# Kernel optimization log

Measured on AMD Instinct MI355X. Metric: run time of the kernel, lower is better.

## Reference

```python
import jax, jax.numpy as jnp
import numpy as np

N = 50000
E = 800000
D = 128
EPS = 1e-5


def setup_inputs() -> dict:
    key = jax.random.key(0)
    ks = jax.random.split(key, 12)
    s1 = 1.0 / np.sqrt(2 * D)
    s2 = 1.0 / np.sqrt(D)
    return {
        "x": jax.random.normal(ks[0], (N, D), dtype=jnp.float32),
        "edge_index": jax.random.randint(ks[1], (2, E), 0, N, dtype=jnp.int32),
        # message MLP: Linear(2D->D), SiLU, Linear(D->D)
        "wm1": jax.random.uniform(ks[2], (2 * D, D), jnp.float32, -s1, s1),
        "bm1": jax.random.uniform(ks[3], (D,), jnp.float32, -s1, s1),
        "wm2": jax.random.uniform(ks[4], (D, D), jnp.float32, -s2, s2),
        "bm2": jax.random.uniform(ks[5], (D,), jnp.float32, -s2, s2),
        # update MLP: Linear(2D->D), SiLU, Linear(D->D)
        "wu1": jax.random.uniform(ks[6], (2 * D, D), jnp.float32, -s1, s1),
        "bu1": jax.random.uniform(ks[7], (D,), jnp.float32, -s1, s1),
        "wu2": jax.random.uniform(ks[8], (D, D), jnp.float32, -s2, s2),
        "bu2": jax.random.uniform(ks[9], (D,), jnp.float32, -s2, s2),
        # LayerNorm affine
        "gamma": jnp.ones((D,), jnp.float32),
        "beta": jnp.zeros((D,), jnp.float32),
    }


def reference(x, edge_index, wm1, bm1, wm2, bm2, wu1, bu1, wu2, bu2, gamma, beta):
    row, col = edge_index[0], edge_index[1]
    # gather endpoints and build message input [E, 2D]
    msg_in = jnp.concatenate([x[row], x[col]], axis=-1)
    h = jax.nn.silu(msg_in @ wm1 + bm1)
    messages = h @ wm2 + bm2  # [E, D]
    # scatter-add aggregate into destination rows
    aggr = jax.ops.segment_sum(messages, row, num_segments=x.shape[0])  # [N, D]
    upd_in = jnp.concatenate([x, aggr], axis=-1)  # [N, 2D]
    u = jax.nn.silu(upd_in @ wu1 + bu1)
    out = u @ wu2 + bu2  # [N, D]
    # residual + LayerNorm
    y = x + out
    mu = jnp.mean(y, axis=-1, keepdims=True)
    var = jnp.var(y, axis=-1, keepdims=True)
    yn = (y - mu) * jax.lax.rsqrt(var + EPS)
    return yn * gamma + beta
```

## Files before the change

kernel.cpp:

```cpp
#include <hip/hip_runtime.h>
#include <hip/hip_bf16.h>

#define NN 50000
#define EE 800000
#define DD 128
#define TILES (EE / 64)
#define NB_SCAN ((NN + 255) / 256)

typedef __attribute__((ext_vector_type(8))) short bf8v;
typedef __attribute__((ext_vector_type(4))) float f4v;
typedef __attribute__((ext_vector_type(4))) unsigned int u4v;

static __device__ __forceinline__ unsigned int bpack2(float lo, float hi) {
    union { __hip_bfloat162 h2; unsigned int u; } c;
    c.h2 = __float22bfloat162_rn(float2{lo, hi});
    return c.u;
}
static __device__ __forceinline__ u4v pack8(f4v a, f4v b) {
    u4v r;
    r[0] = bpack2(a[0], a[1]); r[1] = bpack2(a[2], a[3]);
    r[2] = bpack2(b[0], b[1]); r[3] = bpack2(b[2], b[3]);
    return r;
}
static __device__ __forceinline__ short f2bf_s(float f) {
    union { __hip_bfloat16 h; short s; } c;
    c.h = __float2bfloat16(f);
    return c.s;
}
static __device__ __forceinline__ float bf_lo(unsigned int u) {
    union { unsigned int u; float f; } c; c.u = u << 16; return c.f;
}
static __device__ __forceinline__ float bf_hi(unsigned int u) {
    union { unsigned int u; float f; } c; c.u = u & 0xffff0000u; return c.f;
}
static __device__ __forceinline__ float silu(float v) {
    return v * __builtin_amdgcn_rcpf(1.f + __expf(-v));
}

__global__ __launch_bounds__(256) void make_frags_all(
    const float* __restrict__ wm1, const float* __restrict__ wm2,
    const float* __restrict__ wu1, const float* __restrict__ wu2,
    short* __restrict__ out) {
    int idx = blockIdx.x * 256 + threadIdx.x;
    const float* src; int l;
    if      (idx < 32768) { src = wm1; l = idx; }
    else if (idx < 49152) { src = wm2; l = idx - 32768; }
    else if (idx < 81920) { src = wu1; l = idx - 49152; }
    else                  { src = wu2; l = idx - 81920; }
    int e    = l & 7;
    int lane = (l >> 3) & 63;
    int ntg  = (l >> 9) & 7;
    int kc   = l >> 12;
    out[idx] = f2bf_s(src[(kc * 32 + (lane >> 4) * 8 + e) * DD + ntg * 16 + (lane & 15)]);
}

__global__ __launch_bounds__(256) void hist_rank_kernel(const int* __restrict__ ei,
                                                        int* __restrict__ cnt,
                                                        int* __restrict__ rank) {
    int e = blockIdx.x * 256 + threadIdx.x;
    if (e < EE) rank[e] = atomicAdd(&cnt[ei[e]], 1);
}

__global__ __launch_bounds__(256) void scanA_kernel(const int* __restrict__ cnt,
                                                    int* __restrict__ bsum) {
    __shared__ int sd[256];
    int t = threadIdx.x;
    int i = blockIdx.x * 256 + t;
    sd[t] = (i < NN) ? cnt[i] : 0;
    __syncthreads();
    for (int off = 128; off > 0; off >>= 1) {
        if (t < off) sd[t] += sd[t + off];
        __syncthreads();
    }
    if (t == 0) bsum[blockIdx.x] = sd[0];
}

__global__ __launch_bounds__(256) void scanB_kernel(const int* __restrict__ bsum,
                                                    int* __restrict__ bscan) {
    __shared__ int sd[256];
    int t = threadIdx.x;
    int v = (t < NB_SCAN) ? bsum[t] : 0;
    sd[t] = v;
    __syncthreads();
    for (int off = 1; off < 256; off <<= 1) {
        int u = (t >= off) ? sd[t - off] : 0;
        __syncthreads();
        sd[t] += u;
        __syncthreads();
    }
    if (t < NB_SCAN) bscan[t] = sd[t] - v;
}

__global__ __launch_bounds__(256) void scanC_kernel(const int* __restrict__ cnt,
                                                    const int* __restrict__ bscan,
                                                    int* __restrict__ cursor) {
    __shared__ int sd[256];
    int t = threadIdx.x;
    int i = blockIdx.x * 256 + t;
    int v = (i < NN) ? cnt[i] : 0;
    sd[t] = v;
    __syncthreads();
    for (int off = 1; off < 256; off <<= 1) {
        int u = (t >= off) ? sd[t - off] : 0;
        __syncthreads();
        sd[t] += u;
        __syncthreads();
    }
    if (i < NN) cursor[i] = bscan[blockIdx.x] + sd[t] - v;
}

__global__ __launch_bounds__(256) void scatter_rank_kernel(const int* __restrict__ ei,
                                                           const int* __restrict__ cursor,
                                                           const int* __restrict__ rank,
                                                           int2* __restrict__ srt2) {
    int e = blockIdx.x * 256 + threadIdx.x;
    if (e < EE) {
        int r = ei[e];
        srt2[cursor[r] + rank[e]] = make_int2(r, ei[EE + e]);
    }
}

__global__ __launch_bounds__(256) void scatter_atomic_kernel(const int* __restrict__ ei,
                                                             int* __restrict__ cursor,
                                                             int2* __restrict__ srt2) {
    int e = blockIdx.x * 256 + threadIdx.x;
    if (e < EE) {
        int r = ei[e];
        int pos = atomicAdd(&cursor[r], 1);
        srt2[pos] = make_int2(r, ei[EE + e]);
    }
}

__global__ __launch_bounds__(256) void pq_kernel(
    const float* __restrict__ x,
    const short* __restrict__ W1f, const float* __restrict__ bm1,
    short* __restrict__ P, short* __restrict__ Q)
{
    __shared__ char smem[32768];
    const int tid = threadIdx.x;
    const int w = tid >> 6, lane = tid & 63;
    const int rbase = blockIdx.x * 64;
    const int rloc = tid >> 2, s = tid & 3;

    {
        int rg = rbase + rloc;
        int rgc = rg < NN ? rg : NN - 1;
        const float* xr = x + (size_t)rgc * DD + s * 32;
        int swz = (rloc & 7) << 4;
        #pragma unroll
        for (int j = 0; j < 4; ++j) {
            f4v a0 = *(const f4v*)(xr + j * 8);
            f4v a1 = *(const f4v*)(xr + j * 8 + 4);
            *(u4v*)(smem + ((rloc * 256 + s * 64 + j * 16) ^ swz)) = pack8(a0, a1);
        }
    }

    bf8v w1t[4][2], w1b[4][2];
    #pragma unroll
    for (int kc = 0; kc < 4; ++kc)
        #pragma unroll
        for (int nt = 0; nt < 2; ++nt) {
            w1t[kc][nt] = *(const bf8v*)(W1f + (((kc * 8) + (w * 2 + nt)) * 64 + lane) * 8);
            w1b[kc][nt] = *(const bf8v*)(W1f + ((((kc + 4) * 8) + (w * 2 + nt)) * 64 + lane) * 8);
        }
    __syncthreads();

    f4v accP[4][2], accQ[4][2];
    #pragma unroll
    for (int mt = 0; mt < 4; ++mt)
        #pragma unroll
        for (int nt = 0; nt < 2; ++nt) {
            accP[mt][nt] = (f4v){0.f, 0.f, 0.f, 0.f};
            accQ[mt][nt] = (f4v){0.f, 0.f, 0.f, 0.f};
        }
    #pragma unroll
    for (int kc = 0; kc < 4; ++kc) {
        bf8v a[4];
        int kb = kc * 64 + (lane >> 4) * 16;
        #pragma unroll
        for (int mt = 0; mt < 4; ++mt) {
            int row = mt * 16 + (lane & 15);
            a[mt] = *(const bf8v*)(smem + ((row * 256 + kb) ^ ((row & 7) << 4)));
        }
        #pragma unroll
        for (int mt = 0; mt < 4; ++mt)
            #pragma unroll
            for (int nt = 0; nt < 2; ++nt) {
                accP[mt][nt] = __builtin_amdgcn_mfma_f32_16x16x32_bf16(a[mt], w1t[kc][nt], accP[mt][nt], 0, 0, 0);
                accQ[mt][nt] = __builtin_amdgcn_mfma_f32_16x16x32_bf16(a[mt], w1b[kc][nt], accQ[mt][nt], 0, 0, 0);
            }
    }
    __syncthreads();

    int col0 = w * 32 + (lane & 15);
    float b1a = bm1[col0], b1b = bm1[col0 + 16];
    #pragma unroll
    for (int mt = 0; mt < 4; ++mt)
        #pragma unroll
        for (int nt = 0; nt < 2; ++nt) {
            float bb = nt ? b1b : b1a;
            int col = col0 + nt * 16;
            #pragma unroll
            for (int r = 0; r < 4; ++r) {
                int row = mt * 16 + (lane >> 4) * 4 + r;
                int off = (row * 256 + col * 2) ^ ((row & 7) << 4);
                *(short*)(smem + off)         = f2bf_s(accP[mt][nt][r] + bb);
                *(short*)(smem + 16384 + off) = f2bf_s(accQ[mt][nt][r]);
            }
        }
    __syncthreads();

    {
        int rg = rbase + rloc;
        if (rg < NN) {
            int swz = (rloc & 7) << 4;
            #pragma unroll
            for (int j = 0; j < 4; ++j) {
                int off = (rloc * 256 + s * 64 + j * 16) ^ swz;
                *(u4v*)(P + (size_t)rg * DD + s * 32 + j * 8) = *(const u4v*)(smem + off);
                *(u4v*)(Q + (size_t)rg * DD + s * 32 + j * 8) = *(const u4v*)(smem + 16384 + off);
            }
        }
    }
}

__global__ __launch_bounds__(256, 4) void edge_kernel(
    const short* __restrict__ P, const short* __restrict__ Q,
    const int2* __restrict__ srt2, const int* __restrict__ ei, int use_pairs,
    const short* __restrict__ W2f, const float* __restrict__ bm2,
    float* __restrict__ aggr)
{
    __shared__ char smem[32768 + 256];
    char* Hs = smem;
    char* Ms = smem + 16384;
    int* rows_s = (int*)(smem + 32768);

    const int tid = threadIdx.x;
    const int w = tid >> 6, lane = tid & 63;
    const int rloc = tid >> 2, s = tid & 3;

    {
        int eg = blockIdx.x * 64 + rloc;
        int2 rc = use_pairs ? srt2[eg] : make_int2(ei[eg], ei[EE + eg]);
        if (s == 0) rows_s[rloc] = rc.x;
        const u4v* pr = (const u4v*)(P + (size_t)rc.x * DD + s * 32);
        const u4v* qr = (const u4v*)(Q + (size_t)rc.y * DD + s * 32);
        int swz = (rloc & 7) << 4;
        #pragma unroll
        for (int j = 0; j < 4; ++j) {
            u4v pj = pr[j], qj = qr[j];
            u4v hv;
            #pragma unroll
            for (int k2 = 0; k2 < 4; ++k2) {
                float lo = silu(bf_lo(pj[k2]) + bf_lo(qj[k2]));
                float hi = silu(bf_hi(pj[k2]) + bf_hi(qj[k2]));
                hv[k2] = bpack2(lo, hi);
            }
            *(u4v*)(Hs + ((rloc * 256 + s * 64 + j * 16) ^ swz)) = hv;
        }
    }

    bf8v w2f[4][2];
    #pragma unroll
    for (int kc = 0; kc < 4; ++kc)
        #pragma unroll
        for (int nt = 0; nt < 2; ++nt)
            w2f[kc][nt] = *(const bf8v*)(W2f + (((kc * 8) + (w * 2 + nt)) * 64 + lane) * 8);
    int col0 = w * 32 + (lane & 15);
    float b2a = bm2[col0], b2b = bm2[col0 + 16];

    __syncthreads();

    f4v acc2[4][2];
    #pragma unroll
    for (int mt = 0; mt < 4; ++mt)
        #pragma unroll
        for (int nt = 0; nt < 2; ++nt)
            acc2[mt][nt] = (f4v){0.f, 0.f, 0.f, 0.f};
    #pragma unroll
    for (int kc = 0; kc < 4; ++kc) {
        bf8v a[4];
        int kb = kc * 64 + (lane >> 4) * 16;
        #pragma unroll
        for (int mt = 0; mt < 4; ++mt) {
            int row = mt * 16 + (lane & 15);
            a[mt] = *(const bf8v*)(Hs + ((row * 256 + kb) ^ ((row & 7) << 4)));
        }
        #pragma unroll
        for (int mt = 0; mt < 4; ++mt)
            #pragma unroll
            for (int nt = 0; nt < 2; ++nt)
                acc2[mt][nt] = __builtin_amdgcn_mfma_f32_16x16x32_bf16(a[mt], w2f[kc][nt], acc2[mt][nt], 0, 0, 0);
    }

    #pragma unroll
    for (int mt = 0; mt < 4; ++mt)
        #pragma unroll
        for (int nt = 0; nt < 2; ++nt) {
            int col = col0 + nt * 16;
            float bb = nt ? b2b : b2a;
            #pragma unroll
            for (int r = 0; r < 4; ++r) {
                int row = mt * 16 + (lane >> 4) * 4 + r;
                *(short*)(Ms + ((row * 256 + col * 2) ^ ((row & 7) << 4))) = f2bf_s(acc2[mt][nt][r] + bb);
            }
        }
    __syncthreads();

    {
        int col = tid & 127;
        int r0 = (tid >> 7) * 32;
        int cur = rows_s[r0];
        float run = 0.f;
        for (int k = 0; k < 32; ++k) {
            int row = r0 + k;
            int d = rows_s[row];
            unsigned short sv = *(const unsigned short*)(Ms + ((row * 256 + col * 2) ^ ((row & 7) << 4)));
            union { unsigned int u; float f; } c; c.u = ((unsigned int)sv) << 16;
            if (d != cur) {
                unsafeAtomicAdd(aggr + (size_t)cur * DD + col, run);
                run = 0.f; cur = d;
            }
            run += c.f;
        }
        unsafeAtomicAdd(aggr + (size_t)cur * DD + col, run);
    }
}

__global__ __launch_bounds__(256, 4) void node_kernel(
    const float* __restrict__ x, const float* __restrict__ aggr,
    const short* __restrict__ U1f, const short* __restrict__ U2f,
    const float* __restrict__ bu1, const float* __restrict__ bu2,
    const float* __restrict__ gmm, const float* __restrict__ bta,
    float* __restrict__ out)
{
    __shared__ char smem[64 * 512 + 2048];
    char* As = smem;
    float* ps  = (float*)(smem + 64 * 512);
    float* ps2 = ps + 256;

    const int tid = threadIdx.x;
    const int w = tid >> 6, lane = tid & 63;
    const int rbase = blockIdx.x * 64;

    {
        int rloc = tid >> 2, s = tid & 3;
        int rg = rbase + rloc;
        int rgc = rg < NN ? rg : 0;
        const float* xr = x + (size_t)rgc * DD + s * 32;
        const float* ar = aggr + (size_t)rgc * DD + s * 32;
        int swz = (rloc & 7) << 4;
        #pragma unroll
        for (int i2 = 0; i2 < 4; ++i2) {
            f4v a0 = *(const f4v*)(xr + i2 * 8);
            f4v a1 = *(const f4v*)(xr + i2 * 8 + 4);
            int addr = rloc * 512 + s * 64 + i2 * 16;
            *(u4v*)(As + (addr ^ swz)) = pack8(a0, a1);
            f4v b0 = *(const f4v*)(ar + i2 * 8);
            f4v b1 = *(const f4v*)(ar + i2 * 8 + 4);
            int addr2 = rloc * 512 + 256 + s * 64 + i2 * 16;
            *(u4v*)(As + (addr2 ^ swz)) = pack8(b0, b1);
        }
    }

    bf8v u1f[8][2], u2f[4][2];
    #pragma unroll
    for (int kc = 0; kc < 8; ++kc)
        #pragma unroll
        for (int nt = 0; nt < 2; ++nt)
            u1f[kc][nt] = *(const bf8v*)(U1f + (((kc * 8) + (w * 2 + nt)) * 64 + lane) * 8);
    #pragma unroll
    for (int kc = 0; kc < 4; ++kc)
        #pragma unroll
        for (int nt = 0; nt < 2; ++nt)
            u2f[kc][nt] = *(const bf8v*)(U2f + (((kc * 8) + (w * 2 + nt)) * 64 + lane) * 8);

    __syncthreads();

    f4v acc[4][2];
    #pragma unroll
    for (int mt = 0; mt < 4; ++mt)
        #pragma unroll
        for (int nt = 0; nt < 2; ++nt)
            acc[mt][nt] = (f4v){0.f, 0.f, 0.f, 0.f};
    #pragma unroll
    for (int kc = 0; kc < 8; ++kc) {
        bf8v a[4];
        int kb = kc * 64 + (lane >> 4) * 16;
        #pragma unroll
        for (int mt = 0; mt < 4; ++mt) {
            int row = mt * 16 + (lane & 15);
            a[mt] = *(const bf8v*)(As + ((row * 512 + kb) ^ ((row & 7) << 4)));
        }
        #pragma unroll
        for (int mt = 0; mt < 4; ++mt)
            #pragma unroll
            for (int nt = 0; nt < 2; ++nt)
                acc[mt][nt] = __builtin_amdgcn_mfma_f32_16x16x32_bf16(a[mt], u1f[kc][nt], acc[mt][nt], 0, 0, 0);
    }
    __syncthreads();

    int col0 = w * 32 + (lane & 15);
    float b1a = bu1[col0], b1b = bu1[col0 + 16];
    #pragma unroll
    for (int mt = 0; mt < 4; ++mt)
        #pragma unroll
        for (int nt = 0; nt < 2; ++nt) {
            float bb = nt ? b1b : b1a;
            int col = col0 + nt * 16;
            #pragma unroll
            for (int r = 0; r < 4; ++r) {
                float v = silu(acc[mt][nt][r] + bb);
                int row = mt * 16 + (lane >> 4) * 4 + r;
                *(short*)(As + ((row * 256 + col * 2) ^ ((row & 7) << 4))) = f2bf_s(v);
            }
        }
    __syncthreads();

    f4v acc2[4][2];
    #pragma unroll
    for (int mt = 0; mt < 4; ++mt)
        #pragma unroll
        for (int nt = 0; nt < 2; ++nt)
            acc2[mt][nt] = (f4v){0.f, 0.f, 0.f, 0.f};
    #pragma unroll
    for (int kc = 0; kc < 4; ++kc) {
        bf8v a[4];
        int kb = kc * 64 + (lane >> 4) * 16;
        #pragma unroll
        for (int mt = 0; mt < 4; ++mt) {
            int row = mt * 16 + (lane & 15);
            a[mt] = *(const bf8v*)(As + ((row * 256 + kb) ^ ((row & 7) << 4)));
        }
        #pragma unroll
        for (int mt = 0; mt < 4; ++mt)
            #pragma unroll
            for (int nt = 0; nt < 2; ++nt)
                acc2[mt][nt] = __builtin_amdgcn_mfma_f32_16x16x32_bf16(a[mt], u2f[kc][nt], acc2[mt][nt], 0, 0, 0);
    }
    __syncthreads();

    float b2a = bu2[col0], b2b = bu2[col0 + 16];
    #pragma unroll
    for (int mt = 0; mt < 4; ++mt)
        #pragma unroll
        for (int nt = 0; nt < 2; ++nt) {
            int col = col0 + nt * 16;
            float bb = nt ? b2b : b2a;
            #pragma unroll
            for (int r = 0; r < 4; ++r) {
                int rowl = mt * 16 + (lane >> 4) * 4 + r;
                int rg = rbase + rowl;
                int rgc = rg < NN ? rg : 0;
                float xv = x[(size_t)rgc * DD + col];
                float y = acc2[mt][nt][r] + bb + xv;
                *(float*)(As + ((rowl * 512 + col * 4) ^ ((rowl & 7) << 4))) = y;
            }
        }
    __syncthreads();

    {
        int rloc = tid >> 2, q = tid & 3;
        float s1 = 0.f, s2 = 0.f;
        #pragma unroll
        for (int i = 0; i < 8; ++i) {
            f4v v = *(const f4v*)(As + ((rloc * 512 + q * 128 + i * 16) ^ ((rloc & 7) << 4)));
            s1 += v[0] + v[1] + v[2] + v[3];
            s2 += v[0] * v[0] + v[1] * v[1] + v[2] * v[2] + v[3] * v[3];
        }
        ps[rloc * 4 + q] = s1;
        ps2[rloc * 4 + q] = s2;
    }
    __syncthreads();
    {
        int rloc = tid >> 2, q = tid & 3;
        float fs  = ps[rloc * 4] + ps[rloc * 4 + 1] + ps[rloc * 4 + 2] + ps[rloc * 4 + 3];
        float fs2 = ps2[rloc * 4] + ps2[rloc * 4 + 1] + ps2[rloc * 4 + 2] + ps2[rloc * 4 + 3];
        float mu  = fs * (1.f / 128.f);
        float var = fs2 * (1.f / 128.f) - mu * mu;
        float inv = rsqrtf(var + 1e-5f);
        int rg = rbase + rloc;
        if (rg < NN) {
            #pragma unroll
            for (int i = 0; i < 8; ++i) {
                int col = q * 32 + i * 4;
                f4v v  = *(const f4v*)(As + ((rloc * 512 + col * 4) ^ ((rloc & 7) << 4)));
                f4v gg = *(const f4v*)(gmm + col);
                f4v bb = *(const f4v*)(bta + col);
                f4v o;
                #pragma unroll
                for (int j = 0; j < 4; ++j)
                    o[j] = (v[j] - mu) * inv * gg[j] + bb[j];
                *(f4v*)(out + (size_t)rg * DD + col) = o;
            }
        }
    }
}

extern "C" void kernel_launch(void* const* d_in, const int* in_sizes, int n_in,
                              void* d_out, int out_size, void* d_ws, size_t ws_size,
                              hipStream_t stream) {
    const float* x    = (const float*)d_in[0];
    const int*   ei   = (const int*)d_in[1];
    const float* wm1  = (const float*)d_in[2];
    const float* bm1  = (const float*)d_in[3];
    const float* wm2  = (const float*)d_in[4];
    const float* bm2  = (const float*)d_in[5];
    const float* wu1  = (const float*)d_in[6];
    const float* bu1  = (const float*)d_in[7];
    const float* wu2  = (const float*)d_in[8];
    const float* bu2  = (const float*)d_in[9];
    const float* gmm  = (const float*)d_in[10];
    const float* bta  = (const float*)d_in[11];
    float* out = (float*)d_out;

    const size_t off_P     = 0;
    const size_t off_Q     = 12800000;
    const size_t off_frags = 25600000;
    const size_t off_cnt   = 25796608;
    const size_t off_cur   = 25996608;
    const size_t off_bsum  = 26196608;
    const size_t off_bscan = 26197632;
    const size_t off_srt2  = 26198656;
    const size_t off_rank  = 32598656;
    const size_t need_rank   = 35798656;
    const size_t need_atomic = 32598656;

    char* wsB = (char*)d_ws;
    short* P    = (short*)(wsB + off_P);
    short* Q    = (short*)(wsB + off_Q);
    short* Wf   = (short*)(wsB + off_frags);
    short* W1f  = Wf;
    short* W2f  = Wf + 32768;
    short* U1f  = Wf + 49152;
    short* U2f  = Wf + 81920;
    int*   cnt    = (int*)(wsB + off_cnt);
    int*   cursor = (int*)(wsB + off_cur);
    int*   bsum   = (int*)(wsB + off_bsum);
    int*   bscan  = (int*)(wsB + off_bscan);
    int*   rank   = (int*)(wsB + off_rank);
    int2*  srt2   = (int2*)(wsB + off_srt2);

    float* aggr = (float*)d_out;
    const size_t aggr_b = (size_t)NN * DD * sizeof(float);

    int tier = (ws_size >= need_rank) ? 2 : (ws_size >= need_atomic ? 1 : 0);

    make_frags_all<<<384, 256, 0, stream>>>(wm1, wm2, wu1, wu2, Wf);
    hipMemsetAsync(aggr, 0, aggr_b, stream);
    pq_kernel<<<(NN + 63) / 64, 256, 0, stream>>>(x, W1f, bm1, P, Q);

    int use_pairs = 0;
    if (tier > 0) {
        hipMemsetAsync(cnt, 0, (size_t)NN * 4, stream);
        if (tier == 2) {
            hist_rank_kernel<<<(EE + 255) / 256, 256, 0, stream>>>(ei, cnt, rank);
        } else {
            hist_rank_kernel<<<(EE + 255) / 256, 256, 0, stream>>>(ei, cnt, (int*)srt2);
        }
        scanA_kernel<<<NB_SCAN, 256, 0, stream>>>(cnt, bsum);
        scanB_kernel<<<1, 256, 0, stream>>>(bsum, bscan);
        scanC_kernel<<<NB_SCAN, 256, 0, stream>>>(cnt, bscan, cursor);
        if (tier == 2)
            scatter_rank_kernel<<<(EE + 255) / 256, 256, 0, stream>>>(ei, cursor, rank, srt2);
        else
            scatter_atomic_kernel<<<(EE + 255) / 256, 256, 0, stream>>>(ei, cursor, srt2);
        use_pairs = 1;
    }

    edge_kernel<<<TILES, 256, 0, stream>>>(P, Q, srt2, ei, use_pairs, W2f, bm2, aggr);
    node_kernel<<<(NN + 63) / 64, 256, 0, stream>>>(x, aggr, U1f, U2f, bu1, bu2, gmm, bta, out);
}
```

Baseline: 207.1 us.

## Reuse shared tile for messages, split sorted edge arrays, fuse memsets into setup

The edge kernel now writes its bf16 message tile back into the H buffer after a barrier. This halves its shared memory so the launch bound can allow eight blocks per CU. The sorted edge list is stored as a separate column array plus a row array filled per node by a new kernel, replacing the scattered int2 pairs. The zeroing of counts and the aggregate buffer moves into the weight-fragment setup kernel, removing two memset calls. The trade-offs are an extra barrier, an extra small kernel, and a possible register-pressure increase under the tighter launch bound.

After: 198.1 us. 4.4% less time.

```diff
diff --git a/kernel.cpp b/kernel.cpp
--- a/kernel.cpp
+++ b/kernel.cpp
@@ -37,21 +37,26 @@
     return v * __builtin_amdgcn_rcpf(1.f + __expf(-v));
 }
 
-__global__ __launch_bounds__(256) void make_frags_all(
+__global__ __launch_bounds__(256) void setup_kernel(
     const float* __restrict__ wm1, const float* __restrict__ wm2,
     const float* __restrict__ wu1, const float* __restrict__ wu2,
-    short* __restrict__ out) {
+    short* __restrict__ out, int* __restrict__ cnt, float* __restrict__ aggr) {
     int idx = blockIdx.x * 256 + threadIdx.x;
-    const float* src; int l;
-    if      (idx < 32768) { src = wm1; l = idx; }
-    else if (idx < 49152) { src = wm2; l = idx - 32768; }
-    else if (idx < 81920) { src = wu1; l = idx - 49152; }
-    else                  { src = wu2; l = idx - 81920; }
-    int e    = l & 7;
-    int lane = (l >> 3) & 63;
-    int ntg  = (l >> 9) & 7;
-    int kc   = l >> 12;
-    out[idx] = f2bf_s(src[(kc * 32 + (lane >> 4) * 8 + e) * DD + ntg * 16 + (lane & 15)]);
+    {
+        const float* src; int l;
+        if      (idx < 32768) { src = wm1; l = idx; }
+        else if (idx < 49152) { src = wm2; l = idx - 32768; }
+        else if (idx < 81920) { src = wu1; l = idx - 49152; }
+        else                  { src = wu2; l = idx - 81920; }
+        int e    = l & 7;
+        int lane = (l >> 3) & 63;
+        int ntg  = (l >> 9) & 7;
+        int kc   = l >> 12;
+        out[idx] = f2bf_s(src[(kc * 32 + (lane >> 4) * 8 + e) * DD + ntg * 16 + (lane & 15)]);
+    }
+    for (int i = idx; i < NN; i += 98304) cnt[i] = 0;
+    f4v z = (f4v){0.f, 0.f, 0.f, 0.f};
+    for (int i = idx; i < NN * DD / 4; i += 98304) ((f4v*)aggr)[i] = z;
 }
 
 __global__ __launch_bounds__(256) void hist_rank_kernel(const int* __restrict__ ei,
@@ -109,25 +114,31 @@
     if (i < NN) cursor[i] = bscan[blockIdx.x] + sd[t] - v;
 }
 
-__global__ __launch_bounds__(256) void scatter_rank_kernel(const int* __restrict__ ei,
-                                                           const int* __restrict__ cursor,
-                                                           const int* __restrict__ rank,
-                                                           int2* __restrict__ srt2) {
+__global__ __launch_bounds__(256) void rows_fill_kernel(const int* __restrict__ cursor,
+                                                        const int* __restrict__ cnt,
+                                                        int* __restrict__ rows) {
+    int r = blockIdx.x * 256 + threadIdx.x;
+    if (r < NN) {
+        int b = cursor[r], n = cnt[r];
+        for (int i = 0; i < n; ++i) rows[b + i] = r;
+    }
+}
+
+__global__ __launch_bounds__(256) void scatter_col_rank_kernel(const int* __restrict__ ei,
+                                                               const int* __restrict__ cursor,
+                                                               const int* __restrict__ rank,
+                                                               int* __restrict__ srtc) {
+    int e = blockIdx.x * 256 + threadIdx.x;
+    if (e < EE) srtc[cursor[ei[e]] + rank[e]] = ei[EE + e];
+}
+
+__global__ __launch_bounds__(256) void scatter_col_atomic_kernel(const int* __restrict__ ei,
+                                                                 int* __restrict__ cursor,
+                                                                 int* __restrict__ srtc) {
     int e = blockIdx.x * 256 + threadIdx.x;
     if (e < EE) {
-        int r = ei[e];
-        srt2[cursor[r] + rank[e]] = make_int2(r, ei[EE + e]);
-    }
-}
-
-__global__ __launch_bounds__(256) void scatter_atomic_kernel(const int* __restrict__ ei,
-                                                             int* __restrict__ cursor,
-                                                             int2* __restrict__ srt2) {
-    int e = blockIdx.x * 256 + threadIdx.x;
-    if (e < EE) {
-        int r = ei[e];
-        int pos = atomicAdd(&cursor[r], 1);
-        srt2[pos] = make_int2(r, ei[EE + e]);
+        int pos = atomicAdd(&cursor[ei[e]], 1);
+        srtc[pos] = ei[EE + e];
     }
 }
 
@@ -224,16 +235,16 @@
     }
 }
 
-__global__ __launch_bounds__(256, 4) void edge_kernel(
+__global__ __launch_bounds__(256, 8) void edge_kernel(
     const short* __restrict__ P, const short* __restrict__ Q,
-    const int2* __restrict__ srt2, const int* __restrict__ ei, int use_pairs,
+    const int* __restrict__ rows, const int* __restrict__ srtc,
+    const int* __restrict__ ei, int use_sorted,
     const short* __restrict__ W2f, const float* __restrict__ bm2,
     float* __restrict__ aggr)
 {
-    __shared__ char smem[32768 + 256];
+    __shared__ char smem[16384 + 256];
     char* Hs = smem;
-    char* Ms = smem + 16384;
-    int* rows_s = (int*)(smem + 32768);
+    int* rows_s = (int*)(smem + 16384);
 
     const int tid = threadIdx.x;
     const int w = tid >> 6, lane = tid & 63;
@@ -241,10 +252,12 @@
 
     {
         int eg = blockIdx.x * 64 + rloc;
-        int2 rc = use_pairs ? srt2[eg] : make_int2(ei[eg], ei[EE + eg]);
-        if (s == 0) rows_s[rloc] = rc.x;
-        const u4v* pr = (const u4v*)(P + (size_t)rc.x * DD + s * 32);
-        const u4v* qr = (const u4v*)(Q + (size_t)rc.y * DD + s * 32);
+        int r, c;
+        if (use_sorted) { r = rows[eg]; c = srtc[eg]; }
+        else            { r = ei[eg];   c = ei[EE + eg]; }
+        if (s == 0) rows_s[rloc] = r;
+        const u4v* pr = (const u4v*)(P + (size_t)r * DD + s * 32);
+        const u4v* qr = (const u4v*)(Q + (size_t)c * DD + s * 32);
         int swz = (rloc & 7) << 4;
         #pragma unroll
         for (int j = 0; j < 4; ++j) {
@@ -292,6 +305,7 @@
             for (int nt = 0; nt < 2; ++nt)
                 acc2[mt][nt] = __builtin_amdgcn_mfma_f32_16x16x32_bf16(a[mt], w2f[kc][nt], acc2[mt][nt], 0, 0, 0);
     }
+    __syncthreads();
 
     #pragma unroll
     for (int mt = 0; mt < 4; ++mt)
@@ -302,7 +316,7 @@
             #pragma unroll
             for (int r = 0; r < 4; ++r) {
                 int row = mt * 16 + (lane >> 4) * 4 + r;
-                *(short*)(Ms + ((row * 256 + col * 2) ^ ((row & 7) << 4))) = f2bf_s(acc2[mt][nt][r] + bb);
+                *(short*)(Hs + ((row * 256 + col * 2) ^ ((row & 7) << 4))) = f2bf_s(acc2[mt][nt][r] + bb);
             }
         }
     __syncthreads();
@@ -315,7 +329,7 @@
         for (int k = 0; k < 32; ++k) {
             int row = r0 + k;
             int d = rows_s[row];
-            unsigned short sv = *(const unsigned short*)(Ms + ((row * 256 + col * 2) ^ ((row & 7) << 4)));
+            unsigned short sv = *(const unsigned short*)(Hs + ((row * 256 + col * 2) ^ ((row & 7) << 4)));
             union { unsigned int u; float f; } c; c.u = ((unsigned int)sv) << 16;
             if (d != cur) {
                 unsafeAtomicAdd(aggr + (size_t)cur * DD + col, run);
@@ -521,7 +535,8 @@
     const size_t off_cur   = 25996608;
     const size_t off_bsum  = 26196608;
     const size_t off_bscan = 26197632;
-    const size_t off_srt2  = 26198656;
+    const size_t off_rows  = 26198656;
+    const size_t off_srtc  = 29398656;
     const size_t off_rank  = 32598656;
     const size_t need_rank   = 35798656;
     const size_t need_atomic = 32598656;
@@ -538,36 +553,32 @@
     int*   cursor = (int*)(wsB + off_cur);
     int*   bsum   = (int*)(wsB + off_bsum);
     int*   bscan  = (int*)(wsB + off_bscan);
+    int*   rows   = (int*)(wsB + off_rows);
+    int*   srtc   = (int*)(wsB + off_srtc);
     int*   rank   = (int*)(wsB + off_rank);
-    int2*  srt2   = (int2*)(wsB + off_srt2);
 
     float* aggr = (float*)d_out;
-    const size_t aggr_b = (size_t)NN * DD * sizeof(float);
 
     int tier = (ws_size >= need_rank) ? 2 : (ws_size >= need_atomic ? 1 : 0);
 
-    make_frags_all<<<384, 256, 0, stream>>>(wm1, wm2, wu1, wu2, Wf);
-    hipMemsetAsync(aggr, 0, aggr_b, stream);
+    setup_kernel<<<384, 256, 0, stream>>>(wm1, wm2, wu1, wu2, Wf, cnt, aggr);
     pq_kernel<<<(NN + 63) / 64, 256, 0, stream>>>(x, W1f, bm1, P, Q);
 
-    int use_pairs = 0;
+    int use_sorted = 0;
     if (tier > 0) {
-        hipMemsetAsync(cnt, 0, (size_t)NN * 4, stream);
-        if (tier == 2) {
-            hist_rank_kernel<<<(EE + 255) / 256, 256, 0, stream>>>(ei, cnt, rank);
-        } else {
-            hist_rank_kernel<<<(EE + 255) / 256, 256, 0, stream>>>(ei, cnt, (int*)srt2);
-        }
+        hist_rank_kernel<<<(EE + 255) / 256, 256, 0, stream>>>(ei, cnt,
+            tier == 2 ? rank : srtc );
         scanA_kernel<<<NB_SCAN, 256, 0, stream>>>(cnt, bsum);
         scanB_kernel<<<1, 256, 0, stream>>>(bsum, bscan);
         scanC_kernel<<<NB_SCAN, 256, 0, stream>>>(cnt, bscan, cursor);
+        rows_fill_kernel<<<NB_SCAN, 256, 0, stream>>>(cursor, cnt, rows);
         if (tier == 2)
-            scatter_rank_kernel<<<(EE + 255) / 256, 256, 0, stream>>>(ei, cursor, rank, srt2);
+            scatter_col_rank_kernel<<<(EE + 255) / 256, 256, 0, stream>>>(ei, cursor, rank, srtc);
         else
-            scatter_atomic_kernel<<<(EE + 255) / 256, 256, 0, stream>>>(ei, cursor, srt2);
-        use_pairs = 1;
-    }
-
-    edge_kernel<<<TILES, 256, 0, stream>>>(P, Q, srt2, ei, use_pairs, W2f, bm2, aggr);
+            scatter_col_atomic_kernel<<<(EE + 255) / 256, 256, 0, stream>>>(ei, cursor, srtc);
+        use_sorted = 1;
+    }
+
+    edge_kernel<<<TILES, 256, 0, stream>>>(P, Q, rows, srtc, ei, use_sorted, W2f, bm2, aggr);
     node_kernel<<<(NN + 63) / 64, 256, 0, stream>>>(x, aggr, U1f, U2f, bu1, bu2, gmm, bta, out);
 }
```
